# Kernel optimization log

Hardware: AMD Instinct MI355X
Metric: run time of the kernel (lower is better)

Reference implementation:

```python
import jax, jax.numpy as jnp
import numpy as np
from jax import lax

BN_EPS = 1e-5


def setup_inputs() -> dict:
    key = jax.random.key(0)
    k1, k2 = jax.random.split(key)
    B, C, H, Wd = 32, 256, 56, 56
    x = jax.random.normal(k1, (B, C, H, Wd), dtype=jnp.float32)
    W = jax.random.normal(k2, (C, C, 3, 3), dtype=jnp.float32) * 0.05  # conv weight OIHW
    gamma = jnp.ones((C,), dtype=jnp.float32)
    beta = jnp.zeros((C,), dtype=jnp.float32)
    return {"x": x, "W": W, "gamma": gamma, "beta": beta}


def reference(x, W, gamma, beta):
    # sign activation on input, sign-binarized weights
    s = jnp.sign(x)
    bw = jnp.sign(W)
    # 3x3 conv, stride 1, padding 1 (same spatial size)
    y = lax.conv_general_dilated(
        s, bw,
        window_strides=(1, 1),
        padding=((1, 1), (1, 1)),
        dimension_numbers=("NCHW", "OIHW", "NCHW"),
    )
    # BatchNorm2d in training mode: batch statistics over (N, H, W), biased variance
    mean = jnp.mean(y, axis=(0, 2, 3))
    var = jnp.var(y, axis=(0, 2, 3))
    inv = gamma / jnp.sqrt(var + BN_EPS)
    yn = (y - mean[None, :, None, None]) * inv[None, :, None, None] + beta[None, :, None, None]
    return yn + x
```

## Files before the change

kernel.cpp:

```cpp
#include <hip/hip_runtime.h>
#include <stdint.h>

#define CH 256
#define HWD 56
#define POS 3136
#define BATCH 32
#define PP 3364
#define NCHUNK 51

typedef unsigned long long u64;
typedef __attribute__((ext_vector_type(4))) int  i32x4;
typedef __attribute__((ext_vector_type(16))) int i32x16;
typedef __attribute__((ext_vector_type(8))) short short8;

#define GLL16(gsrc, ldst) \
    __builtin_amdgcn_global_load_lds((const __attribute__((address_space(1))) void*)(gsrc), \
                                     (__attribute__((address_space(3))) void*)(ldst), 16, 0, 0)

__global__ __launch_bounds__(256) void pack_kernel(
        const float* __restrict__ x, const float* __restrict__ W,
        char* __restrict__ Xp, char* __restrict__ Wb2){
    int blk = blockIdx.x, t = threadIdx.x;
    if (blk < 144){
        int idx = blk*256 + t;
        int cc = idx & 15;
        int ot = idx >> 4;
        int o = ot / 9, tap = ot % 9;
        char v16[16];
        #pragma unroll
        for (int j=0;j<16;j++){
            float v = W[(size_t)(o*CH + cc*16 + j)*9 + tap];
            v16[j] = (v >= 0.f) ? 1 : -1;
        }
        *(int4*)(Wb2 + ((size_t)(tap*16 + cc)*256 + o)*16) = *(int4*)v16;
        return;
    }
    int xb = blk - 144;
    int h = xb % 56, b = xb / 56;
    __shared__ char lds[56][256];
    int wave = t >> 6, l = t & 63;
    for (int i = 0; i < 64; ++i){
        int c = wave*64 + i;
        if (l < 56){
            float v = x[((size_t)(b*CH + c))*POS + h*HWD + l];
            lds[l][c ^ ((l & 31) << 2)] = (v >= 0.f) ? (char)1 : (char)-1;
        }
    }
    __syncthreads();
    #pragma unroll
    for (int i = 0; i < 4; ++i){
        int idx = t + 256*i;
        if (idx < 896){
            int cc = idx & 15, w = idx >> 4;
            int swz = (w & 31) << 2;
            int4 val;
            val.x = *(const int*)&lds[w][(cc*16 + 0) ^ swz];
            val.y = *(const int*)&lds[w][(cc*16 + 4) ^ swz];
            val.z = *(const int*)&lds[w][(cc*16 + 8) ^ swz];
            val.w = *(const int*)&lds[w][(cc*16 +12) ^ swz];
            int n = b*PP + (h+1)*58 + (w+1);
            *(int4*)(Xp + (size_t)n*256 + ((cc ^ (n & 15)) << 4)) = val;
        }
    }
}

__global__ __launch_bounds__(512, 4) void conv_kernel(
        const char* __restrict__ Xp, const char* __restrict__ Wb2,
        short* __restrict__ y16, int* __restrict__ sumI, u64* __restrict__ sumQ){
    __shared__ char BL[184*256];
    __shared__ int sS[256], sQ[256];
    int blk = blockIdx.x;
    int b = blk / NCHUNK, chunk = blk - b*NCHUNK;
    int n0 = b*PP + 58 + chunk*64;
    int t = threadIdx.x;
    int wave = t >> 6, l = t & 63;
    int half = l >> 5, l31 = l & 31;

    const char* src = Xp + (size_t)(n0 - 59)*256;
    #pragma unroll
    for (int i=0;i<6;++i){
        int idx = t + 512*i;
        if (idx < 2944) GLL16(src + (size_t)idx*16, BL + idx*16);
    }
    if (t < 256){ sS[t]=0; sQ[t]=0; }
    __syncthreads();

    i32x16 acc[2];
    #pragma unroll
    for (int nt=0;nt<2;++nt)
        #pragma unroll
        for (int r=0;r<16;++r) acc[nt][r] = 0;

    int c0 = (n0 - 59) & 15;

    #pragma unroll 1
    for (int tap=0; tap<9; ++tap){
        int dh = tap/3 - 1, dw = tap%3 - 1;
        int off = dh*58 + dw;
        const char* wt = Wb2 + (size_t)tap*65536 + (size_t)(half*256 + wave*32 + l31)*16;
        i32x4 afr[8];
        #pragma unroll
        for (int ks=0; ks<8; ++ks)
            afr[ks] = *(const i32x4*)(wt + ks*8192);
        #pragma unroll
        for (int nt=0; nt<2; ++nt){
            int s = 59 + nt*32 + l31 + off;
            int key = (s + c0) & 15;
            int sb = s << 8;
            #pragma unroll
            for (int ks=0; ks<8; ++ks){
                int kch = ks*2 + half;
                i32x4 bfr = *(const i32x4*)(BL + sb + ((kch ^ key) << 4));
                acc[nt] = __builtin_amdgcn_mfma_i32_32x32x32_i8(afr[ks], bfr, acc[nt], 0,0,0);
            }
        }
    }

    #pragma unroll
    for (int nt=0; nt<2; ++nt){
        unsigned nloc = 58 + chunk*64 + nt*32 + l31;
        unsigned hq = nloc / 58;
        unsigned wq = nloc - hq*58;
        bool vok = (hq <= 56) && (wq >= 1) && (wq <= 56);
        size_t pbase = (size_t)(hq-1)*HWD + (wq-1);
        #pragma unroll
        for (int reg=0; reg<16; ++reg){
            int o = wave*32 + (reg&3) + 8*(reg>>2) + 4*half;
            int v = acc[nt][reg];
            if (vok) y16[(size_t)(b*CH + o)*POS + pbase] = (short)v;
            int s_ = vok ? v : 0;
            int q_ = vok ? v*v : 0;
            #pragma unroll
            for (int mk=1; mk<32; mk<<=1){
                s_ += __shfl_xor(s_, mk);
                q_ += __shfl_xor(q_, mk);
            }
            if (l31 == 0){
                atomicAdd(&sS[o], s_);
                atomicAdd(&sQ[o], q_);
            }
        }
    }
    __syncthreads();
    if (t < 256){
        atomicAdd(&sumI[t], sS[t]);
        atomicAdd(&sumQ[t], (u64)(unsigned)sQ[t]);
    }
}

__global__ void apply_kernel(const short* __restrict__ y16, const float* __restrict__ x,
                             const int* __restrict__ sumI, const u64* __restrict__ sumQ,
                             const float* __restrict__ gamma, const float* __restrict__ beta,
                             float* __restrict__ out){
    int t = blockIdx.x*blockDim.x + threadIdx.x;
    const int total8 = BATCH*CH*POS/8;
    if (t >= total8) return;
    size_t i = (size_t)t*8;
    int c = (t / (POS/8)) & 255;

    const double N = (double)(BATCH*POS);
    double mean = (double)sumI[c] / N;
    double msq  = (double)sumQ[c] / N;
    double var  = msq - mean*mean;
    double inv  = (double)gamma[c] / sqrt(var + 1e-5);
    float iv = (float)inv;
    float sh = (float)((double)beta[c] - mean*inv);

    short8 yv = *(const short8*)(y16 + i);
    float4 x0 = *(const float4*)(x + i);
    float4 x1 = *(const float4*)(x + i + 4);
    float4 o0, o1;
    o0.x = fmaf((float)yv[0], iv, sh) + x0.x;
    o0.y = fmaf((float)yv[1], iv, sh) + x0.y;
    o0.z = fmaf((float)yv[2], iv, sh) + x0.z;
    o0.w = fmaf((float)yv[3], iv, sh) + x0.w;
    o1.x = fmaf((float)yv[4], iv, sh) + x1.x;
    o1.y = fmaf((float)yv[5], iv, sh) + x1.y;
    o1.z = fmaf((float)yv[6], iv, sh) + x1.z;
    o1.w = fmaf((float)yv[7], iv, sh) + x1.w;
    *(float4*)(out + i)     = o0;
    *(float4*)(out + i + 4) = o1;
}

extern "C" void kernel_launch(void* const* d_in, const int* in_sizes, int n_in,
                              void* d_out, int out_size, void* d_ws, size_t ws_size,
                              hipStream_t stream) {
    const float* x     = (const float*)d_in[0];
    const float* W     = (const float*)d_in[1];
    const float* gamma = (const float*)d_in[2];
    const float* beta  = (const float*)d_in[3];
    float* out = (float*)d_out;

    char* ws = (char*)d_ws;
    short* y16   = (short*)ws;
    int*   sumI  = (int*)(ws + 51380224);
    u64*   sumQ  = (u64*)(ws + 51381248);
    char*  Wb2   = (char*)(ws + 51383296);

    char* Xp = (char*)d_out + 64*256;

    hipMemsetAsync(d_out, 0, (size_t)(107648 + 128)*256, stream);
    hipMemsetAsync(sumI, 0, 3072, stream);

    pack_kernel<<<144 + BATCH*HWD, 256, 0, stream>>>(x, W, Xp, Wb2);
    conv_kernel<<<BATCH*NCHUNK, 512, 0, stream>>>(Xp, Wb2, y16, sumI, sumQ);
    apply_kernel<<<(BATCH*CH*POS/8 + 255)/256, 256, 0, stream>>>(y16, x, sumI, sumQ, gamma, beta, out);
}
```

Measured before the change: 327.0 us.

## Enlarge conv tile to 128 positions, split stats into separate kernel, vectorize pack

The conv kernel now processes 128 spatial positions per block, with each wave computing a 64x64 output tile (two M fragments sharing each B fragment). This reuses every LDS B read for two MFMAs and halves redundant halo loads. The per-channel sum and sum-of-squares reductions (shuffles plus atomics) move out of the conv epilogue into a separate stats kernel that rereads y16. The pack kernel now loads x with float4 instead of scalar loads. The trade-offs are an extra pass over the int16 intermediate, a larger LDS footprint and more registers, which lowers occupancy.

```diff
diff --git a/kernel.cpp b/kernel.cpp
--- a/kernel.cpp
+++ b/kernel.cpp
@@ -6,7 +6,8 @@
 #define POS 3136
 #define BATCH 32
 #define PP 3364
-#define NCHUNK 51
+#define BN 128
+#define NCH 26
 
 typedef unsigned long long u64;
 typedef __attribute__((ext_vector_type(4))) int  i32x4;
@@ -38,13 +39,16 @@
     int xb = blk - 144;
     int h = xb % 56, b = xb / 56;
     __shared__ char lds[56][256];
-    int wave = t >> 6, l = t & 63;
-    for (int i = 0; i < 64; ++i){
-        int c = wave*64 + i;
-        if (l < 56){
-            float v = x[((size_t)(b*CH + c))*POS + h*HWD + l];
-            lds[l][c ^ ((l & 31) << 2)] = (v >= 0.f) ? (char)1 : (char)-1;
-        }
+    #pragma unroll
+    for (int i = 0; i < 14; ++i){
+        int idx = i*256 + t;
+        int c = idx / 14, wq = idx - c*14;
+        float4 v = *(const float4*)(x + ((size_t)(b*CH + c))*POS + h*HWD + wq*4);
+        int w0 = wq*4;
+        lds[w0+0][c ^ (((w0+0) & 31) << 2)] = (v.x >= 0.f) ? (char)1 : (char)-1;
+        lds[w0+1][c ^ (((w0+1) & 31) << 2)] = (v.y >= 0.f) ? (char)1 : (char)-1;
+        lds[w0+2][c ^ (((w0+2) & 31) << 2)] = (v.z >= 0.f) ? (char)1 : (char)-1;
+        lds[w0+3][c ^ (((w0+3) & 31) << 2)] = (v.w >= 0.f) ? (char)1 : (char)-1;
     }
     __syncthreads();
     #pragma unroll
@@ -64,87 +68,105 @@
     }
 }
 
-__global__ __launch_bounds__(512, 4) void conv_kernel(
+__global__ __launch_bounds__(512) void conv_kernel(
         const char* __restrict__ Xp, const char* __restrict__ Wb2,
-        short* __restrict__ y16, int* __restrict__ sumI, u64* __restrict__ sumQ){
-    __shared__ char BL[184*256];
-    __shared__ int sS[256], sQ[256];
+        short* __restrict__ y16){
+    __shared__ char BL[256*256];
     int blk = blockIdx.x;
-    int b = blk / NCHUNK, chunk = blk - b*NCHUNK;
-    int n0 = b*PP + 58 + chunk*64;
+    int b = blk / NCH, chunk = blk - b*NCH;
+    int n0 = b*PP + 58 + chunk*BN;
     int t = threadIdx.x;
     int wave = t >> 6, l = t & 63;
+    int gm = wave & 3, gn = wave >> 2;
     int half = l >> 5, l31 = l & 31;
 
-    const char* src = Xp + (size_t)(n0 - 59)*256;
-    #pragma unroll
-    for (int i=0;i<6;++i){
+    const char* src = Xp + (size_t)(n0 - 64)*256;
+    #pragma unroll
+    for (int i=0;i<8;++i){
         int idx = t + 512*i;
-        if (idx < 2944) GLL16(src + (size_t)idx*16, BL + idx*16);
-    }
-    if (t < 256){ sS[t]=0; sQ[t]=0; }
+        GLL16(src + (size_t)idx*16, BL + idx*16);
+    }
     __syncthreads();
 
-    i32x16 acc[2];
-    #pragma unroll
-    for (int nt=0;nt<2;++nt)
-        #pragma unroll
-        for (int r=0;r<16;++r) acc[nt][r] = 0;
-
-    int c0 = (n0 - 59) & 15;
+    i32x16 acc[2][2];
+    #pragma unroll
+    for (int m=0;m<2;++m)
+        #pragma unroll
+        for (int nt=0;nt<2;++nt)
+            #pragma unroll
+            for (int r=0;r<16;++r) acc[m][nt][r] = 0;
+
+    int c0 = (n0 - 64) & 15;
 
     #pragma unroll 1
     for (int tap=0; tap<9; ++tap){
-        int dh = tap/3 - 1, dw = tap%3 - 1;
-        int off = dh*58 + dw;
-        const char* wt = Wb2 + (size_t)tap*65536 + (size_t)(half*256 + wave*32 + l31)*16;
-        i32x4 afr[8];
-        #pragma unroll
-        for (int ks=0; ks<8; ++ks)
-            afr[ks] = *(const i32x4*)(wt + ks*8192);
+        int off = (tap/3 - 1)*58 + (tap%3 - 1);
+        const char* wt = Wb2 + (size_t)tap*65536 + (size_t)half*4096
+                             + (size_t)(gm*64 + l31)*16;
+        i32x4 afr[2][8];
+        #pragma unroll
+        for (int m=0;m<2;++m)
+            #pragma unroll
+            for (int ks=0; ks<8; ++ks)
+                afr[m][ks] = *(const i32x4*)(wt + m*512 + ks*8192);
         #pragma unroll
         for (int nt=0; nt<2; ++nt){
-            int s = 59 + nt*32 + l31 + off;
+            int s = 64 + gn*64 + nt*32 + l31 + off;
             int key = (s + c0) & 15;
-            int sb = s << 8;
+            const char* bb = BL + (s << 8);
             #pragma unroll
             for (int ks=0; ks<8; ++ks){
-                int kch = ks*2 + half;
-                i32x4 bfr = *(const i32x4*)(BL + sb + ((kch ^ key) << 4));
-                acc[nt] = __builtin_amdgcn_mfma_i32_32x32x32_i8(afr[ks], bfr, acc[nt], 0,0,0);
+                i32x4 bfr = *(const i32x4*)(bb + (((2*ks + half) ^ key) << 4));
+                acc[0][nt] = __builtin_amdgcn_mfma_i32_32x32x32_i8(afr[0][ks], bfr, acc[0][nt], 0,0,0);
+                acc[1][nt] = __builtin_amdgcn_mfma_i32_32x32x32_i8(afr[1][ks], bfr, acc[1][nt], 0,0,0);
             }
         }
     }
 
     #pragma unroll
     for (int nt=0; nt<2; ++nt){
-        unsigned nloc = 58 + chunk*64 + nt*32 + l31;
+        unsigned nloc = 58 + chunk*BN + gn*64 + nt*32 + l31;
         unsigned hq = nloc / 58;
         unsigned wq = nloc - hq*58;
         bool vok = (hq <= 56) && (wq >= 1) && (wq <= 56);
+        if (!vok) continue;
         size_t pbase = (size_t)(hq-1)*HWD + (wq-1);
         #pragma unroll
-        for (int reg=0; reg<16; ++reg){
-            int o = wave*32 + (reg&3) + 8*(reg>>2) + 4*half;
-            int v = acc[nt][reg];
-            if (vok) y16[(size_t)(b*CH + o)*POS + pbase] = (short)v;
-            int s_ = vok ? v : 0;
-            int q_ = vok ? v*v : 0;
-            #pragma unroll
-            for (int mk=1; mk<32; mk<<=1){
-                s_ += __shfl_xor(s_, mk);
-                q_ += __shfl_xor(q_, mk);
+        for (int m=0;m<2;++m){
+            #pragma unroll
+            for (int reg=0; reg<16; ++reg){
+                int o = gm*64 + m*32 + (reg&3) + 8*(reg>>2) + 4*half;
+                y16[(size_t)(b*CH + o)*POS + pbase] = (short)acc[m][nt][reg];
             }
-            if (l31 == 0){
-                atomicAdd(&sS[o], s_);
-                atomicAdd(&sQ[o], q_);
-            }
-        }
-    }
+        }
+    }
+}
+
+__global__ __launch_bounds__(256) void stats_kernel(const short* __restrict__ y16,
+                                                    int* __restrict__ sumI, u64* __restrict__ sumQ){
+    int o = blockIdx.x, t = threadIdx.x;
+    int s = 0; unsigned q = 0;
+    for (int b=0; b<BATCH; ++b){
+        const short8* yp = (const short8*)(y16 + ((size_t)(b*CH + o))*POS);
+        for (int i=t; i<POS/8; i+=256){
+            short8 v = yp[i];
+            #pragma unroll
+            for (int j=0;j<8;++j){ int vv = v[j]; s += vv; q += (unsigned)(vv*vv); }
+        }
+    }
+    long long ls = s, lq = (long long)q;
+    #pragma unroll
+    for (int off=32; off; off>>=1){
+        ls += __shfl_xor(ls, off);
+        lq += __shfl_xor(lq, off);
+    }
+    __shared__ long long wsum[4], wsq[4];
+    int wave = t >> 6, lane = t & 63;
+    if (lane == 0){ wsum[wave] = ls; wsq[wave] = lq; }
     __syncthreads();
-    if (t < 256){
-        atomicAdd(&sumI[t], sS[t]);
-        atomicAdd(&sumQ[t], (u64)(unsigned)sQ[t]);
+    if (t == 0){
+        sumI[o] = (int)(wsum[0]+wsum[1]+wsum[2]+wsum[3]);
+        sumQ[o] = (u64)(wsq[0]+wsq[1]+wsq[2]+wsq[3]);
     }
 }
 
@@ -193,16 +215,16 @@
 
     char* ws = (char*)d_ws;
     short* y16   = (short*)ws;
-    int*   sumI  = (int*)(ws + 51380224);
-    u64*   sumQ  = (u64*)(ws + 51381248);
-    char*  Wb2   = (char*)(ws + 51383296);
+    char*  Wb2   = (char*)(ws + 51380224);
+    int*   sumI  = (int*)(ws + 51970048);
+    u64*   sumQ  = (u64*)(ws + 51971072);
 
     char* Xp = (char*)d_out + 64*256;
 
-    hipMemsetAsync(d_out, 0, (size_t)(107648 + 128)*256, stream);
-    hipMemsetAsync(sumI, 0, 3072, stream);
+    hipMemsetAsync(d_out, 0, (size_t)(64 + 107648 + 128)*256, stream);
 
     pack_kernel<<<144 + BATCH*HWD, 256, 0, stream>>>(x, W, Xp, Wb2);
-    conv_kernel<<<BATCH*NCHUNK, 512, 0, stream>>>(Xp, Wb2, y16, sumI, sumQ);
+    conv_kernel<<<BATCH*NCH, 512, 0, stream>>>(Xp, Wb2, y16);
+    stats_kernel<<<CH, 256, 0, stream>>>(y16, sumI, sumQ);
     apply_kernel<<<(BATCH*CH*POS/8 + 255)/256, 256, 0, stream>>>(y16, x, sumI, sumQ, gamma, beta, out);
 }
```

After: 315.7 us. 3.5% less time.
